# Kernel optimization log

Hardware: AMD Instinct MI355X
Metric: run time of the kernel (lower is better)

The kernel has to match this reference:

```python
import jax, jax.numpy as jnp
import numpy as np

NUM_USERS = 100000
NUM_PROTO = 16
EMBD_DIM = 128
BATCH = 8192
SEQ = 50
MOMENTUM = 0.9


def _l2norm(x, axis=-1, eps=1e-12):
    # matches torch F.normalize: x / max(||x||, eps)
    n = jnp.linalg.norm(x, axis=axis, keepdims=True)
    return x / jnp.maximum(n, eps)


def setup_inputs() -> dict:
    key = jax.random.key(0)
    k1, k2, k3, k4, k5 = jax.random.split(key, 5)
    user_idx = jnp.arange(BATCH, dtype=jnp.int64 if jax.config.jax_enable_x64 else jnp.int32)
    features = jax.random.normal(k1, (BATCH, SEQ, EMBD_DIM), dtype=jnp.float32)
    success_mask = jax.random.uniform(k2, (BATCH, SEQ), dtype=jnp.float32)
    user_prototypes = jax.random.normal(k3, (NUM_USERS, NUM_PROTO, EMBD_DIM), dtype=jnp.float32)
    shared_prototypes = jax.random.normal(k4, (1, NUM_PROTO, EMBD_DIM), dtype=jnp.float32)
    interaction_count = jax.random.uniform(k5, (NUM_USERS,), dtype=jnp.float32) * 500.0
    return {
        "user_idx": user_idx,
        "features": features,
        "success_mask": success_mask,
        "user_prototypes": user_prototypes,
        "shared_prototypes": shared_prototypes,
        "interaction_count": interaction_count,
    }


def reference(user_idx, features, success_mask, user_prototypes, shared_prototypes, interaction_count):
    # ---- get_prototypes: gather + curriculum blend ----
    cnt = interaction_count[user_idx]                          # [B]
    w = jax.nn.sigmoid(cnt / 100.0 - 3.0)[:, None, None]       # [B,1,1]
    user_p = user_prototypes[user_idx]                         # [B,P,D] gather
    combined = w * user_p + (1.0 - w) * shared_prototypes      # [B,P,D]

    # ---- update_prototypes: momentum blend + normalize + scatter ----
    m = jnp.clip(MOMENTUM + cnt / 1000.0, MOMENTUM, 0.99)[:, None, None]  # [B,1,1]
    sm = success_mask[..., None]                               # [B,S,1]
    masked = features * sm                                     # [B,S,D]
    denom = jnp.maximum(jnp.sum(sm, axis=1), 1e-6)             # [B,1]
    upd = jnp.sum(masked, axis=1) / denom                      # [B,D]
    upd = _l2norm(upd)                                         # [B,D]
    upd_b = jnp.broadcast_to(upd[:, None, :], (upd.shape[0], NUM_PROTO, upd.shape[1]))  # [B,P,D]

    new_rows = m * user_p + (1.0 - m) * upd_b                  # [B,P,D]
    new_user_prototypes = user_prototypes.at[user_idx].set(new_rows)  # scatter write-back

    shared_upd = _l2norm(jnp.mean(upd_b, axis=0))              # [P,D]
    new_shared = MOMENTUM * shared_prototypes + (1.0 - MOMENTUM) * shared_upd[None]  # [1,P,D]

    new_interaction_count = interaction_count.at[user_idx].add(1.0)
    return combined, new_rows, new_user_prototypes, new_shared, new_interaction_count
```

## Files before the change

kernel.cpp:

```cpp
#include <hip/hip_runtime.h>

#define BATCH   8192
#define SEQ     50
#define DIM     128
#define NPROTO  16
#define NUSERS  100000
#define ROWF4   (NPROTO * DIM / 4)
#define DF4     (DIM / 4)

typedef float vf4 __attribute__((ext_vector_type(4)));

__global__ void k_init(const float* __restrict__ icount, int* __restrict__ inv,
                       float* __restrict__ out_count) {
    int i = blockIdx.x * blockDim.x + threadIdx.x;
    if (i < NUSERS) {
        inv[i] = -1;
        out_count[i] = icount[i];
    }
}

__global__ void k_prep(const int* __restrict__ idx, int* __restrict__ inv,
                       float* __restrict__ out_count) {
    int b = blockIdx.x * blockDim.x + threadIdx.x;
    if (b >= BATCH) return;
    int u = idx[b];
    inv[u] = b;
    atomicAdd(&out_count[u], 1.0f);
}

__global__ void __launch_bounds__(256) k_mega(
        const int* __restrict__ idx, const int* __restrict__ inv,
        const float* __restrict__ icount,
        const float* __restrict__ feat, const float* __restrict__ mask,
        const vf4* __restrict__ userP, const vf4* __restrict__ sharedP,
        float* __restrict__ upd,
        vf4* __restrict__ out1, vf4* __restrict__ out2, vf4* __restrict__ out3) {
    int bid = blockIdx.x;
    int t = threadIdx.x;

    if (bid >= BATCH) {
        int u = bid - BATCH;
        if (inv[u] >= 0) return;
        size_t base = (size_t)u * ROWF4;
        #pragma unroll
        for (int k = 0; k < 2; ++k) {
            int i = t + k * 256;
            vf4 v = __builtin_nontemporal_load(&userP[base + i]);
            __builtin_nontemporal_store(v, &out3[base + i]);
        }
        return;
    }

    int b = bid;
    int u = idx[b];

    __shared__ vf4  lds_acc[8][32];
    __shared__ float lds_m[8];
    __shared__ vf4  lds_upd[32];

    int l = t & 31;
    int g = t >> 5;
    const vf4* f4p = (const vf4*)(feat + (size_t)b * SEQ * DIM);
    const float* mk = mask + (size_t)b * SEQ;
    vf4 acc = {0.f, 0.f, 0.f, 0.f};
    float msum = 0.f;
    for (int s = g; s < SEQ; s += 8) {
        float m = mk[s];
        acc += __builtin_nontemporal_load(&f4p[s * DF4 + l]) * m;
        msum += m;
    }
    lds_acc[g][l] = acc;
    if (l == 0) lds_m[g] = msum;
    __syncthreads();
    if (t < 32) {
        vf4 a = lds_acc[0][t];
        #pragma unroll
        for (int gg = 1; gg < 8; ++gg) a += lds_acc[gg][t];
        float ms = lds_m[0];
        #pragma unroll
        for (int gg = 1; gg < 8; ++gg) ms += lds_m[gg];
        a *= 1.0f / fmaxf(ms, 1e-6f);
        float sq = a.x*a.x + a.y*a.y + a.z*a.z + a.w*a.w;
        for (int off = 16; off >= 1; off >>= 1)
            sq += __shfl_xor(sq, off, 32);
        a *= 1.0f / fmaxf(sqrtf(sq), 1e-12f);
        lds_upd[t] = a;
        ((vf4*)(upd + (size_t)b * DIM))[t] = a;
    }
    __syncthreads();

    float cnt = icount[u];
    float w = 1.0f / (1.0f + expf(3.0f - cnt * 0.01f));
    float m = fminf(fmaxf(0.9f + cnt * 0.001f, 0.9f), 0.99f);
    float w1 = 1.0f - w, m1 = 1.0f - m;
    size_t base = (size_t)u * ROWF4;
    size_t ob   = (size_t)b * ROWF4;
    #pragma unroll
    for (int k = 0; k < 2; ++k) {
        int i = t + k * 256;
        vf4 p  = __builtin_nontemporal_load(&userP[base + i]);
        vf4 sh = sharedP[i];
        vf4 ud = lds_upd[i & (DF4 - 1)];
        vf4 c  = w * p + w1 * sh;
        vf4 nr = m * p + m1 * ud;
        __builtin_nontemporal_store(c,  &out1[ob + i]);
        __builtin_nontemporal_store(nr, &out2[ob + i]);
        __builtin_nontemporal_store(nr, &out3[base + i]);
    }
}

__global__ void k_partial(const float* __restrict__ upd, float* __restrict__ part) {
    int d = threadIdx.x;
    int j = blockIdx.x;
    float acc = 0.f;
    for (int b = j; b < BATCH; b += 128)
        acc += upd[(size_t)b * DIM + d];
    part[j * DIM + d] = acc;
}

__global__ void k_shared(const float* __restrict__ part, const float* __restrict__ sharedP,
                         float* __restrict__ out4) {
    __shared__ float red[DIM];
    int d = threadIdx.x;
    float s = 0.f;
    for (int j = 0; j < 128; ++j) s += part[j * DIM + d];
    float mean = s * (1.0f / (float)BATCH);
    red[d] = mean * mean;
    __syncthreads();
    for (int off = 64; off >= 1; off >>= 1) {
        if (d < off) red[d] += red[d + off];
        __syncthreads();
    }
    float normed = mean / fmaxf(sqrtf(red[0]), 1e-12f);
    for (int p = 0; p < NPROTO; ++p)
        out4[p * DIM + d] = 0.9f * sharedP[p * DIM + d] + 0.1f * normed;
}

extern "C" void kernel_launch(void* const* d_in, const int* in_sizes, int n_in,
                              void* d_out, int out_size, void* d_ws, size_t ws_size,
                              hipStream_t stream) {
    const int*   user_idx = (const int*)d_in[0];
    const float* features = (const float*)d_in[1];
    const float* smask    = (const float*)d_in[2];
    const float* userP    = (const float*)d_in[3];
    const float* sharedP  = (const float*)d_in[4];
    const float* icount   = (const float*)d_in[5];

    float* out = (float*)d_out;
    const size_t n1 = (size_t)BATCH * NPROTO * DIM;
    const size_t n3 = (size_t)NUSERS * NPROTO * DIM;
    float* out_combined = out;
    float* out_newrows  = out + n1;
    float* out_newproto = out + 2 * n1;
    float* out_shared   = out + 2 * n1 + n3;
    float* out_count    = out_shared + (size_t)NPROTO * DIM;

    float* ws_upd  = (float*)d_ws;
    float* ws_part = ws_upd + (size_t)BATCH * DIM;
    int*   ws_inv  = (int*)(ws_part + 128 * DIM);

    k_init<<<(NUSERS + 255) / 256, 256, 0, stream>>>(icount, ws_inv, out_count);
    k_prep<<<(BATCH + 255) / 256, 256, 0, stream>>>(user_idx, ws_inv, out_count);
    k_mega<<<BATCH + NUSERS, 256, 0, stream>>>(user_idx, ws_inv, icount,
                                               features, smask,
                                               (const vf4*)userP, (const vf4*)sharedP,
                                               ws_upd,
                                               (vf4*)out_combined, (vf4*)out_newrows,
                                               (vf4*)out_newproto);
    k_partial<<<128, 128, 0, stream>>>(ws_upd, ws_part);
    k_shared<<<1, 128, 0, stream>>>(ws_part, sharedP, out_shared);
}
```

Measured before the change: 356.1 us.

## Batch copy blocks per four users, fold count update into copy, fuse shared reduction

After: 372.3 us. 1.05x slower.

```diff
diff --git a/kernel.cpp b/kernel.cpp
--- a/kernel.cpp
+++ b/kernel.cpp
@@ -7,25 +7,20 @@
 #define NUSERS  100000
 #define ROWF4   (NPROTO * DIM / 4)
 #define DF4     (DIM / 4)
+#define UPB     4
+#define NCOPY   (NUSERS / UPB)
 
 typedef float vf4 __attribute__((ext_vector_type(4)));
 
-__global__ void k_init(const float* __restrict__ icount, int* __restrict__ inv,
-                       float* __restrict__ out_count) {
+__global__ void k_init(int* __restrict__ inv, int* __restrict__ counter) {
     int i = blockIdx.x * blockDim.x + threadIdx.x;
-    if (i < NUSERS) {
-        inv[i] = -1;
-        out_count[i] = icount[i];
-    }
+    if (i < NUSERS) inv[i] = -1;
+    if (i == 0) *counter = 0;
 }
 
-__global__ void k_prep(const int* __restrict__ idx, int* __restrict__ inv,
-                       float* __restrict__ out_count) {
+__global__ void k_prep(const int* __restrict__ idx, int* __restrict__ inv) {
     int b = blockIdx.x * blockDim.x + threadIdx.x;
-    if (b >= BATCH) return;
-    int u = idx[b];
-    inv[u] = b;
-    atomicAdd(&out_count[u], 1.0f);
+    if (b < BATCH) inv[idx[b]] = b;
 }
 
 __global__ void __launch_bounds__(256) k_mega(
@@ -33,20 +28,27 @@
         const float* __restrict__ icount,
         const float* __restrict__ feat, const float* __restrict__ mask,
         const vf4* __restrict__ userP, const vf4* __restrict__ sharedP,
-        float* __restrict__ upd,
+        float* __restrict__ upd, float* __restrict__ out_count,
         vf4* __restrict__ out1, vf4* __restrict__ out2, vf4* __restrict__ out3) {
     int bid = blockIdx.x;
     int t = threadIdx.x;
 
     if (bid >= BATCH) {
-        int u = bid - BATCH;
-        if (inv[u] >= 0) return;
-        size_t base = (size_t)u * ROWF4;
+        int u0 = (bid - BATCH) * UPB;
+        const int* ivp = inv + u0;
+        int iv[UPB];
         #pragma unroll
-        for (int k = 0; k < 2; ++k) {
-            int i = t + k * 256;
-            vf4 v = __builtin_nontemporal_load(&userP[base + i]);
-            __builtin_nontemporal_store(v, &out3[base + i]);
+        for (int r = 0; r < UPB; ++r) iv[r] = ivp[r];
+        if (t < UPB)
+            out_count[u0 + t] = icount[u0 + t] + (iv[t] >= 0 ? 1.0f : 0.0f);
+        #pragma unroll
+        for (int r = 0; r < UPB; ++r) {
+            if (iv[r] >= 0) continue;
+            size_t base = (size_t)(u0 + r) * ROWF4;
+            vf4 v0 = __builtin_nontemporal_load(&userP[base + t]);
+            vf4 v1 = __builtin_nontemporal_load(&userP[base + t + 256]);
+            __builtin_nontemporal_store(v0, &out3[base + t]);
+            __builtin_nontemporal_store(v1, &out3[base + t + 256]);
         }
         return;
     }
@@ -109,21 +111,25 @@
     }
 }
 
-__global__ void k_partial(const float* __restrict__ upd, float* __restrict__ part) {
+__global__ void k_shared_fused(const float* __restrict__ upd, const float* __restrict__ sharedP,
+                               float* __restrict__ out4, float* __restrict__ part,
+                               int* __restrict__ counter) {
+    __shared__ float red[DIM];
+    __shared__ int s_ticket;
     int d = threadIdx.x;
     int j = blockIdx.x;
     float acc = 0.f;
     for (int b = j; b < BATCH; b += 128)
         acc += upd[(size_t)b * DIM + d];
     part[j * DIM + d] = acc;
-}
-
-__global__ void k_shared(const float* __restrict__ part, const float* __restrict__ sharedP,
-                         float* __restrict__ out4) {
-    __shared__ float red[DIM];
-    int d = threadIdx.x;
+    __threadfence();
+    __syncthreads();
+    if (d == 0) s_ticket = atomicAdd(counter, 1);
+    __syncthreads();
+    if (s_ticket != 127) return;
+    __threadfence();
     float s = 0.f;
-    for (int j = 0; j < 128; ++j) s += part[j * DIM + d];
+    for (int jj = 0; jj < 128; ++jj) s += part[jj * DIM + d];
     float mean = s * (1.0f / (float)BATCH);
     red[d] = mean * mean;
     __syncthreads();
@@ -158,15 +164,15 @@
     float* ws_upd  = (float*)d_ws;
     float* ws_part = ws_upd + (size_t)BATCH * DIM;
     int*   ws_inv  = (int*)(ws_part + 128 * DIM);
+    int*   ws_ctr  = ws_inv + NUSERS;
 
-    k_init<<<(NUSERS + 255) / 256, 256, 0, stream>>>(icount, ws_inv, out_count);
-    k_prep<<<(BATCH + 255) / 256, 256, 0, stream>>>(user_idx, ws_inv, out_count);
-    k_mega<<<BATCH + NUSERS, 256, 0, stream>>>(user_idx, ws_inv, icount,
-                                               features, smask,
-                                               (const vf4*)userP, (const vf4*)sharedP,
-                                               ws_upd,
-                                               (vf4*)out_combined, (vf4*)out_newrows,
-                                               (vf4*)out_newproto);
-    k_partial<<<128, 128, 0, stream>>>(ws_upd, ws_part);
-    k_shared<<<1, 128, 0, stream>>>(ws_part, sharedP, out_shared);
+    k_init<<<(NUSERS + 255) / 256, 256, 0, stream>>>(ws_inv, ws_ctr);
+    k_prep<<<(BATCH + 255) / 256, 256, 0, stream>>>(user_idx, ws_inv);
+    k_mega<<<BATCH + NCOPY, 256, 0, stream>>>(user_idx, ws_inv, icount,
+                                              features, smask,
+                                              (const vf4*)userP, (const vf4*)sharedP,
+                                              ws_upd, out_count,
+                                              (vf4*)out_combined, (vf4*)out_newrows,
+                                              (vf4*)out_newproto);
+    k_shared_fused<<<128, 128, 0, stream>>>(ws_upd, sharedP, out_shared, ws_part, ws_ctr);
 }
```
